# Optimization experiments

Hardware: AMD Instinct MI355X
Metric: run time of the kernel (lower is better)

Reference implementation:

```python
import jax, jax.numpy as jnp
import numpy as np

B, T, D, H, NL, DFF = 8, 255, 1024, 16, 8, 4096
DH = D // H
STD = 0.02


def setup_inputs() -> dict:
    key = jax.random.key(0)
    ks = jax.random.split(key, 16)
    n = lambda k, shape, s=STD: jax.random.normal(k, shape, dtype=jnp.float32) * s
    return {
        "x": n(ks[0], (B, T, D), 1.0),
        "mask": jnp.ones((B, T), dtype=jnp.int64),
        "is_train": 0,
        "sum_emb": n(ks[1], (1, D)),
        "modality_emb": n(ks[2], (T + 1, D)),
        "ln1_w": jnp.ones((NL, D), jnp.float32),
        "ln1_b": jnp.zeros((NL, D), jnp.float32),
        "w_qkv": n(ks[3], (NL, D, 3 * D)),
        "b_qkv": jnp.zeros((NL, 3 * D), jnp.float32),
        "w_proj": n(ks[4], (NL, D, D), STD / np.sqrt(2 * NL)),
        "b_proj": jnp.zeros((NL, D), jnp.float32),
        "ln2_w": jnp.ones((NL, D), jnp.float32),
        "ln2_b": jnp.zeros((NL, D), jnp.float32),
        "w_fc": n(ks[5], (NL, D, DFF)),
        "b_fc": jnp.zeros((NL, DFF), jnp.float32),
        "w_out": n(ks[6], (NL, DFF, D), STD / np.sqrt(2 * NL)),
        "b_out": jnp.zeros((NL, D), jnp.float32),
        "norm_w": jnp.ones((D,), jnp.float32),
        "norm_b": jnp.zeros((D,), jnp.float32),
    }


def _ln(x, w, b, eps=1e-5):
    m = x.mean(-1, keepdims=True)
    v = ((x - m) ** 2).mean(-1, keepdims=True)
    return (x - m) / jnp.sqrt(v + eps) * w + b


def reference(x, mask, is_train, sum_emb, modality_emb, ln1_w, ln1_b, w_qkv, b_qkv,
              w_proj, b_proj, ln2_w, ln2_b, w_fc, b_fc, w_out, b_out, norm_w, norm_b):
    b, t, d = x.shape
    L = t + 1
    # prepend summary token + its mask bit, add modality (position) embedding
    summ = jnp.broadcast_to(sum_emb[None, :, :], (b, 1, d))
    h = jnp.concatenate([summ, x], axis=1) + modality_emb[None, :, :]  # [B,L,D]
    full_mask = jnp.concatenate([jnp.ones((b, 1), mask.dtype), mask], axis=1)  # [B,L]
    key_bias = jnp.where(full_mask[:, None, None, :] == 1, 0.0, -1e9)  # [B,1,1,L]
    # is_train==0: random input-drop loop is a no-op in eval mode

    def block(h, p):
        l1w, l1b, wq, bq, wp, bp, l2w, l2b, wf, bf, wo, bo = p
        a = _ln(h, l1w, l1b)
        qkv = a @ wq + bq
        q, k, v = jnp.split(qkv, 3, axis=-1)
        q = q.reshape(b, L, H, DH).transpose(0, 2, 1, 3)
        k = k.reshape(b, L, H, DH).transpose(0, 2, 1, 3)
        v = v.reshape(b, L, H, DH).transpose(0, 2, 1, 3)
        scores = jnp.einsum("bhqd,bhkd->bhqk", q, k) / np.sqrt(DH) + key_bias
        att = jax.nn.softmax(scores, axis=-1)  # [B,H,L,L]
        y = jnp.einsum("bhqk,bhkd->bhqd", att, v).transpose(0, 2, 1, 3).reshape(b, L, d)
        h = h + y @ wp + bp
        m = _ln(h, l2w, l2b)
        h = h + jax.nn.gelu(m @ wf + bf) @ wo + bo
        return h, att

    params = (ln1_w, ln1_b, w_qkv, b_qkv, w_proj, b_proj, ln2_w, ln2_b, w_fc, b_fc, w_out, b_out)
    h, all_att = jax.lax.scan(block, h, params)
    h = _ln(h, norm_w, norm_b)
    return h[:, 0], all_att
```

## Files before the change

kernel.cpp:

```cpp
#include <hip/hip_runtime.h>


using u16 = unsigned short;
typedef __attribute__((ext_vector_type(8))) __bf16 bf16x8;
typedef __attribute__((ext_vector_type(4))) float f32x4;
typedef __attribute__((ext_vector_type(8))) unsigned short ushort8;

__device__ __forceinline__ u16 f2b(float f) {
  unsigned u = __builtin_bit_cast(unsigned, f);
  return (u16)((u + 0x7FFFu + ((u >> 16) & 1u)) >> 16);
}

__device__ __forceinline__ bf16x8 ldfrag(const u16* p) {
  return *reinterpret_cast<const bf16x8*>(p);
}

__device__ __forceinline__ f32x4 mfma16(bf16x8 a, bf16x8 b, f32x4 c) {
  return __builtin_amdgcn_mfma_f32_16x16x32_bf16(a, b, c, 0, 0, 0);
}

__device__ __forceinline__ void gload16(const void* g, void* l) {
  __builtin_amdgcn_global_load_lds(
      (const __attribute__((address_space(1))) unsigned int*)g,
      (__attribute__((address_space(3))) unsigned int*)l, 16, 0, 0);
}

__global__ __launch_bounds__(256) void embed_k(
    const float* __restrict__ x, const float* __restrict__ sum_emb,
    const float* __restrict__ mod_emb, float* __restrict__ h) {
  int idx = blockIdx.x * 256 + threadIdx.x;
  int d = idx & 1023;
  int l = (idx >> 10) & 255;
  int b = idx >> 18;
  float v = (l == 0) ? sum_emb[d] : x[(size_t)(b * 255 + l - 1) * 1024 + d];
  h[idx] = v + mod_emb[l * 1024 + d];
}

__global__ __launch_bounds__(256) void transpose_w(
    const float* __restrict__ in, u16* __restrict__ out, int R, int C) {
  __shared__ float tile[32][33];
  in += (size_t)blockIdx.z * R * C;
  out += (size_t)blockIdx.z * R * C;
  const int t = threadIdx.x;
  const int r0 = blockIdx.y * 32, c0 = blockIdx.x * 32;
  const int tr = t >> 5, tc = t & 31;
#pragma unroll
  for (int i = 0; i < 4; ++i)
    tile[tr + i * 8][tc] = in[(size_t)(r0 + tr + i * 8) * C + c0 + tc];
  __syncthreads();
#pragma unroll
  for (int i = 0; i < 4; ++i) {
    int cc = tr + i * 8, rr = tc;
    out[(size_t)(c0 + cc) * R + r0 + rr] = f2b(tile[rr][cc]);
  }
}

__global__ __launch_bounds__(256) void ln_bf16(
    const float* __restrict__ x, const float* __restrict__ w,
    const float* __restrict__ bb, u16* __restrict__ out) {
  const int r = blockIdx.x, t = threadIdx.x;
  const float* xr = x + (size_t)r * 1024;
  float v[4], s1 = 0.f, s2 = 0.f;
#pragma unroll
  for (int i = 0; i < 4; ++i) {
    v[i] = xr[t + i * 256];
    s1 += v[i];
    s2 += v[i] * v[i];
  }
#pragma unroll
  for (int o = 32; o > 0; o >>= 1) {
    s1 += __shfl_down(s1, o);
    s2 += __shfl_down(s2, o);
  }
  __shared__ float red[8];
  const int wv = t >> 6, l = t & 63;
  if (l == 0) { red[wv] = s1; red[4 + wv] = s2; }
  __syncthreads();
  s1 = red[0] + red[1] + red[2] + red[3];
  s2 = red[4] + red[5] + red[6] + red[7];
  float mean = s1 * (1.0f / 1024.0f);
  float var = s2 * (1.0f / 1024.0f) - mean * mean;
  float rstd = rsqrtf(var + 1e-5f);
#pragma unroll
  for (int i = 0; i < 4; ++i) {
    int c = t + i * 256;
    out[(size_t)r * 1024 + c] = f2b((v[i] - mean) * rstd * w[c] + bb[c]);
  }
}

__global__ __launch_bounds__(256) void final_ln(
    const float* __restrict__ h, const float* __restrict__ w,
    const float* __restrict__ bb, float* __restrict__ out) {
  const int r = blockIdx.x, t = threadIdx.x;
  const float* xr = h + (size_t)r * 262144;
  float v[4], s1 = 0.f, s2 = 0.f;
#pragma unroll
  for (int i = 0; i < 4; ++i) {
    v[i] = xr[t + i * 256];
    s1 += v[i];
    s2 += v[i] * v[i];
  }
#pragma unroll
  for (int o = 32; o > 0; o >>= 1) {
    s1 += __shfl_down(s1, o);
    s2 += __shfl_down(s2, o);
  }
  __shared__ float red[8];
  const int wv = t >> 6, l = t & 63;
  if (l == 0) { red[wv] = s1; red[4 + wv] = s2; }
  __syncthreads();
  s1 = red[0] + red[1] + red[2] + red[3];
  s2 = red[4] + red[5] + red[6] + red[7];
  float mean = s1 * (1.0f / 1024.0f);
  float var = s2 * (1.0f / 1024.0f) - mean * mean;
  float rstd = rsqrtf(var + 1e-5f);
#pragma unroll
  for (int i = 0; i < 4; ++i) {
    int c = t + i * 256;
    out[r * 1024 + c] = (v[i] - mean) * rstd * w[c] + bb[c];
  }
}

template <int EPI, int SPLIT>
__global__ __launch_bounds__(256) void gemm_bt(
    const u16* __restrict__ A, const u16* __restrict__ BT,
    const float* __restrict__ bias, float* __restrict__ Hres,
    u16* __restrict__ Obf, int M, int N, int K) {
  __shared__ u16 As[128 * 32];
  __shared__ u16 Bs[128 * 32];
  const int t = threadIdx.x;
  const int m0 = blockIdx.y * 128, n0 = blockIdx.x * 128;
  const int Kl = K / SPLIT;
  const int kz = (SPLIT > 1) ? blockIdx.z : 0;
  A += (size_t)kz * Kl;
  BT += (size_t)kz * Kl;
  const int l = t & 63, w = t >> 6;
  const int wr = (w >> 1) * 64, wc = (w & 1) * 64;
  const int lr = l & 15, lh = l >> 4;

  const int srow = t >> 2;
  const int skc = (t & 3) * 8;
  const u16* Ag = A + (size_t)(m0 + srow) * K + skc;
  const u16* Bg = BT + (size_t)(n0 + srow) * K + skc;

  f32x4 acc[4][4] = {};
  const int nk = Kl / 32;
  for (int kt = 0; kt < nk; ++kt) {
    __syncthreads();
    gload16(Ag, As + t * 8);
    gload16(Ag + (size_t)64 * K, As + 2048 + t * 8);
    gload16(Bg, Bs + t * 8);
    gload16(Bg + (size_t)64 * K, Bs + 2048 + t * 8);
    Ag += 32;
    Bg += 32;
    __syncthreads();
    bf16x8 af[4], bfr[4];
#pragma unroll
    for (int m = 0; m < 4; ++m) af[m] = ldfrag(As + (wr + m * 16 + lr) * 32 + lh * 8);
#pragma unroll
    for (int n = 0; n < 4; ++n) bfr[n] = ldfrag(Bs + (wc + n * 16 + lr) * 32 + lh * 8);
#pragma unroll
    for (int m = 0; m < 4; ++m)
#pragma unroll
      for (int n = 0; n < 4; ++n) acc[m][n] = mfma16(af[m], bfr[n], acc[m][n]);
  }
#pragma unroll
  for (int m = 0; m < 4; ++m) {
#pragma unroll
    for (int n = 0; n < 4; ++n) {
      const int col = n0 + wc + n * 16 + lr;
      const float bc = (SPLIT == 1 || kz == 0) ? bias[col] : 0.0f;
#pragma unroll
      for (int j = 0; j < 4; ++j) {
        const int row = m0 + wr + m * 16 + lh * 4 + j;
        float v = acc[m][n][j] + bc;
        if (EPI == 0) {
          Obf[(size_t)row * N + col] = f2b(v);
        } else if (EPI == 1) {
          size_t idx = (size_t)row * N + col;
          if (SPLIT == 1) Hres[idx] = Hres[idx] + v;
          else atomicAdd(Hres + idx, v);
        } else {
          float g = 0.5f * v *
                    (1.0f + tanhf(0.7978845608028654f * (v + 0.044715f * v * v * v)));
          Obf[(size_t)row * N + col] = f2b(g);
        }
      }
    }
  }
}

#define VS 264
__device__ __forceinline__ int sfi(int row, int col) {
  return row * 256 + ((col & 7) | (((col >> 3) ^ (row & 7)) << 3));
}

__global__ __launch_bounds__(256) void attn_fused(
    const u16* __restrict__ qkv, const int* __restrict__ mask,
    float* __restrict__ att_out, u16* __restrict__ y) {
  __shared__ u16 Qs[32 * 64];
  __shared__ u16 KV[64 * VS];
  __shared__ float Sf[32 * 256];
  __shared__ float mbias[256];
  __shared__ float rmax[32], rsum[32];
  const int t = threadIdx.x;
  const int blk = blockIdx.x;
  const int qt = blk & 7, hh = (blk >> 3) & 15, b = blk >> 7;
  const int q0 = qt * 32;

  mbias[t] = (t == 0) ? 0.0f : ((mask[b * 255 + t - 1] == 1) ? 0.0f : -1e9f);

  {
    int row = t >> 3, c = t & 7;
    int gcol = (c ^ (row & 7)) * 8;
    gload16(qkv + (size_t)(b * 256 + q0 + row) * 3072 + hh * 64 + gcol, Qs + t * 8);
  }
#pragma unroll
  for (int s = 0; s < 8; ++s) {
    int row = s * 32 + (t >> 3), c = t & 7;
    int gcol = (c ^ (row & 7)) * 8;
    gload16(qkv + (size_t)(b * 256 + row) * 3072 + 1024 + hh * 64 + gcol,
            KV + s * 2048 + t * 8);
  }
  __syncthreads();

  const int l = t & 63, w = t >> 6;
  const int lr = l & 15, lh = l >> 4;
  {
    const int c0 = w * 64;
    f32x4 acc[2][4] = {};
#pragma unroll
    for (int ks = 0; ks < 2; ++ks) {
      bf16x8 af[2], bfr[4];
#pragma unroll
      for (int m = 0; m < 2; ++m) {
        int row = m * 16 + lr;
        int chunk = (ks * 4 + lh) ^ (row & 7);
        af[m] = ldfrag(Qs + row * 64 + chunk * 8);
      }
#pragma unroll
      for (int n = 0; n < 4; ++n) {
        int row = c0 + n * 16 + lr;
        int chunk = (ks * 4 + lh) ^ (row & 7);
        bfr[n] = ldfrag(KV + row * 64 + chunk * 8);
      }
#pragma unroll
      for (int m = 0; m < 2; ++m)
#pragma unroll
        for (int n = 0; n < 4; ++n) acc[m][n] = mfma16(af[m], bfr[n], acc[m][n]);
    }
#pragma unroll
    for (int m = 0; m < 2; ++m)
#pragma unroll
      for (int n = 0; n < 4; ++n) {
        const int col = c0 + n * 16 + lr;
        const float mb = mbias[col];
#pragma unroll
        for (int j = 0; j < 4; ++j) {
          int row = m * 16 + lh * 4 + j;
          Sf[sfi(row, col)] = acc[m][n][j] * 0.125f + mb;
        }
      }
  }
  __syncthreads();

  ushort8 vreg[4][2];
#pragma unroll
  for (int s = 0; s < 4; ++s) {
    const int j = s * 64 + (t >> 2);
    const u16* vsrc =
        qkv + (size_t)(b * 256 + j) * 3072 + 2048 + hh * 64 + (t & 3) * 16;
    vreg[s][0] = *reinterpret_cast<const ushort8*>(vsrc);
    vreg[s][1] = *reinterpret_cast<const ushort8*>(vsrc + 8);
  }

  {
    const int row = t >> 3, tg = t & 7;
    float mx = -1e30f;
#pragma unroll 8
    for (int k = 0; k < 32; ++k) mx = fmaxf(mx, Sf[sfi(row, tg * 32 + k)]);
    mx = fmaxf(mx, __shfl_xor(mx, 1));
    mx = fmaxf(mx, __shfl_xor(mx, 2));
    mx = fmaxf(mx, __shfl_xor(mx, 4));
    float sm = 0.f;
#pragma unroll 8
    for (int k = 0; k < 32; ++k) sm += __expf(Sf[sfi(row, tg * 32 + k)] - mx);
    sm += __shfl_xor(sm, 1);
    sm += __shfl_xor(sm, 2);
    sm += __shfl_xor(sm, 4);
    if (tg == 0) {
      rmax[row] = mx;
      rsum[row] = 1.0f / sm;
    }
  }

#pragma unroll
  for (int s = 0; s < 4; ++s) {
    const int j = s * 64 + (t >> 2);
    const int d0 = (t & 3) * 16;
#pragma unroll
    for (int e = 0; e < 8; ++e) {
      KV[(d0 + e) * VS + j] = vreg[s][0][e];
      KV[(d0 + 8 + e) * VS + j] = vreg[s][1][e];
    }
  }
  __syncthreads();

  const size_t obase = ((size_t)b * 16 + hh) * 65536 + (size_t)q0 * 256;
#pragma unroll 4
  for (int i = 0; i < 32; ++i) {
    float p = __expf(Sf[sfi(i, t)] - rmax[i]) * rsum[i];
    att_out[obase + (size_t)i * 256 + t] = p;
  }

  {
    const int mrow = (w & 1) * 16;
    const int n0c = (w >> 1) * 32;
    const int rr = mrow + lr;
    const float mxl = rmax[rr], rsl = rsum[rr];
    f32x4 acc2[2] = {};
#pragma unroll
    for (int ks = 0; ks < 8; ++ks) {
      const int kbase = ks * 32 + lh * 8;
      const int ch = (kbase >> 3) ^ (rr & 7);
      const float* sp = &Sf[rr * 256 + ch * 8];
      f32x4 s0 = *reinterpret_cast<const f32x4*>(sp);
      f32x4 s1 = *reinterpret_cast<const f32x4*>(sp + 4);
      ushort8 pu;
#pragma unroll
      for (int e = 0; e < 4; ++e) pu[e] = f2b(__expf(s0[e] - mxl) * rsl);
#pragma unroll
      for (int e = 0; e < 4; ++e) pu[4 + e] = f2b(__expf(s1[e] - mxl) * rsl);
      bf16x8 af = __builtin_bit_cast(bf16x8, pu);
#pragma unroll
      for (int n = 0; n < 2; ++n) {
        bf16x8 bfr = ldfrag(KV + (n0c + n * 16 + lr) * VS + kbase);
        acc2[n] = mfma16(af, bfr, acc2[n]);
      }
    }
#pragma unroll
    for (int n = 0; n < 2; ++n)
#pragma unroll
      for (int j = 0; j < 4; ++j) {
        int row = mrow + lh * 4 + j;
        int col = n0c + n * 16 + lr;
        y[(size_t)(b * 256 + q0 + row) * 1024 + hh * 64 + col] = f2b(acc2[n][j]);
      }
  }
}

extern "C" void kernel_launch(void* const* d_in, const int* in_sizes, int n_in,
                              void* d_out, int out_size, void* d_ws, size_t ws_size,
                              hipStream_t stream) {
  (void)in_sizes; (void)n_in; (void)out_size;
  const float* x      = (const float*)d_in[0];
  const int* mask     = (const int*)d_in[1];
  const float* sum_emb = (const float*)d_in[3];
  const float* mod_emb = (const float*)d_in[4];
  const float* ln1_w  = (const float*)d_in[5];
  const float* ln1_b  = (const float*)d_in[6];
  const float* w_qkv  = (const float*)d_in[7];
  const float* b_qkv  = (const float*)d_in[8];
  const float* w_proj = (const float*)d_in[9];
  const float* b_proj = (const float*)d_in[10];
  const float* ln2_w  = (const float*)d_in[11];
  const float* ln2_b  = (const float*)d_in[12];
  const float* w_fc   = (const float*)d_in[13];
  const float* b_fc   = (const float*)d_in[14];
  const float* w_out  = (const float*)d_in[15];
  const float* b_out  = (const float*)d_in[16];
  const float* norm_w = (const float*)d_in[17];
  const float* norm_b = (const float*)d_in[18];

  char* ws = (char*)d_ws;
  float* h    = (float*)(ws + 0);
  u16* a_bf   = (u16*)(ws + 8388608);
  u16* qkv_bf = (u16*)(ws + 12582912);
  u16* y_bf   = (u16*)(ws + 25165824);
  u16* g_bf   = (u16*)(ws + 29360128);
  u16* wqkvT  = (u16*)(ws + 46137344);
  u16* wprojT = (u16*)(ws + 96468992);
  u16* wfcT   = (u16*)(ws + 113246208);
  u16* woutT  = (u16*)(ws + 180355072);
  float* att_f = (float*)d_out + 8192;

  const bool big = ws_size >= 248000000ull;
  const size_t stq = big ? (size_t)3072 * 1024 : 0;
  const size_t stp = big ? (size_t)1024 * 1024 : 0;
  const size_t stf = big ? (size_t)4096 * 1024 : 0;
  const size_t sto = big ? (size_t)4096 * 1024 : 0;

  embed_k<<<8192, 256, 0, stream>>>(x, sum_emb, mod_emb, h);

  if (big) {
    transpose_w<<<dim3(96, 32, 8), 256, 0, stream>>>(w_qkv, wqkvT, 1024, 3072);
    transpose_w<<<dim3(32, 32, 8), 256, 0, stream>>>(w_proj, wprojT, 1024, 1024);
    transpose_w<<<dim3(128, 32, 8), 256, 0, stream>>>(w_fc, wfcT, 1024, 4096);
    transpose_w<<<dim3(32, 128, 8), 256, 0, stream>>>(w_out, woutT, 4096, 1024);
  }

  for (int L = 0; L < 8; ++L) {
    if (!big) {
      transpose_w<<<dim3(96, 32, 1), 256, 0, stream>>>(
          w_qkv + (size_t)L * 1024 * 3072, wqkvT, 1024, 3072);
      transpose_w<<<dim3(32, 32, 1), 256, 0, stream>>>(
          w_proj + (size_t)L * 1024 * 1024, wprojT, 1024, 1024);
      transpose_w<<<dim3(128, 32, 1), 256, 0, stream>>>(
          w_fc + (size_t)L * 1024 * 4096, wfcT, 1024, 4096);
      transpose_w<<<dim3(32, 128, 1), 256, 0, stream>>>(
          w_out + (size_t)L * 4096 * 1024, woutT, 4096, 1024);
    }
    ln_bf16<<<2048, 256, 0, stream>>>(h, ln1_w + L * 1024, ln1_b + L * 1024, a_bf);
    gemm_bt<0, 1><<<dim3(24, 16, 1), 256, 0, stream>>>(
        a_bf, wqkvT + L * stq, b_qkv + L * 3072, nullptr, qkv_bf, 2048, 3072, 1024);
    attn_fused<<<1024, 256, 0, stream>>>(qkv_bf, mask,
                                         att_f + (size_t)L * 8388608, y_bf);
    gemm_bt<1, 2><<<dim3(8, 16, 2), 256, 0, stream>>>(
        y_bf, wprojT + L * stp, b_proj + L * 1024, h, nullptr, 2048, 1024, 1024);
    ln_bf16<<<2048, 256, 0, stream>>>(h, ln2_w + L * 1024, ln2_b + L * 1024, a_bf);
    gemm_bt<2, 1><<<dim3(32, 16, 1), 256, 0, stream>>>(
        a_bf, wfcT + L * stf, b_fc + L * 4096, nullptr, g_bf, 2048, 4096, 1024);
    gemm_bt<1, 4><<<dim3(8, 16, 4), 256, 0, stream>>>(
        g_bf, woutT + L * sto, b_out + L * 1024, h, nullptr, 2048, 1024, 4096);
  }

  final_ln<<<8, 256, 0, stream>>>(h, norm_w, norm_b, (float*)d_out);
}
```

Before: 2.110 ms.

## Rewrite GEMM with double-buffered LDS, 128x256 tiles, XOR swizzle and grid remap

The GEMM kernel is replaced by a 512-thread version that computes 128x256 output tiles with a K-step of 64. It double-buffers the LDS tiles so the next tile's global-to-LDS loads overlap the current MFMAs, and drops one barrier per iteration. Shared-memory columns are XOR-swizzled to avoid bank conflicts, and block IDs are remapped in groups of 8 for better cache locality. The proj GEMM moves from split-K 2 to split-K 4, which means more atomics. The larger tiles also raise LDS use to about 96KB and reduce the number of blocks per GEMM.

```diff
diff --git a/kernel.cpp b/kernel.cpp
--- a/kernel.cpp
+++ b/kernel.cpp
@@ -122,57 +122,84 @@
 }
 
 template <int EPI, int SPLIT>
-__global__ __launch_bounds__(256) void gemm_bt(
+__global__ __launch_bounds__(512) void gemm2p(
     const u16* __restrict__ A, const u16* __restrict__ BT,
     const float* __restrict__ bias, float* __restrict__ Hres,
     u16* __restrict__ Obf, int M, int N, int K) {
-  __shared__ u16 As[128 * 32];
-  __shared__ u16 Bs[128 * 32];
+  __shared__ u16 As[2][128 * 64];
+  __shared__ u16 Bs[2][256 * 64];
   const int t = threadIdx.x;
-  const int m0 = blockIdx.y * 128, n0 = blockIdx.x * 128;
+  const int gx = gridDim.x, nwg = gx * gridDim.y;
+  int id = blockIdx.y * gx + blockIdx.x;
+  id = (id & 7) * (nwg >> 3) + (id >> 3);
+  const int m0 = (id / gx) * 128, n0 = (id % gx) * 256;
+
   const int Kl = K / SPLIT;
   const int kz = (SPLIT > 1) ? blockIdx.z : 0;
   A += (size_t)kz * Kl;
   BT += (size_t)kz * Kl;
+
   const int l = t & 63, w = t >> 6;
-  const int wr = (w >> 1) * 64, wc = (w & 1) * 64;
+  const int wm = w >> 2, wn = w & 3;
   const int lr = l & 15, lh = l >> 4;
 
-  const int srow = t >> 2;
-  const int skc = (t & 3) * 8;
-  const u16* Ag = A + (size_t)(m0 + srow) * K + skc;
-  const u16* Bg = BT + (size_t)(n0 + srow) * K + skc;
+  const int sr = t >> 3, sc = t & 7;
+  const int scA = (sc ^ (sr & 7)) * 8;
 
   f32x4 acc[4][4] = {};
-  const int nk = Kl / 32;
+  const int nk = Kl / 64;
+  int cur = 0;
+
+#define STAGE_TILE(bb, kt)                                                     \
+  {                                                                            \
+    const size_t kof = (size_t)(kt)*64 + scA;                                  \
+    gload16(A + (size_t)(m0 + sr) * K + kof, &As[bb][t * 8]);                  \
+    gload16(A + (size_t)(m0 + sr + 64) * K + kof, &As[bb][4096 + t * 8]);      \
+    gload16(BT + (size_t)(n0 + sr) * K + kof, &Bs[bb][t * 8]);                 \
+    gload16(BT + (size_t)(n0 + sr + 64) * K + kof, &Bs[bb][4096 + t * 8]);     \
+    gload16(BT + (size_t)(n0 + sr + 128) * K + kof, &Bs[bb][8192 + t * 8]);    \
+    gload16(BT + (size_t)(n0 + sr + 192) * K + kof, &Bs[bb][12288 + t * 8]);   \
+  }
+
+  STAGE_TILE(0, 0);
+  __syncthreads();
+
   for (int kt = 0; kt < nk; ++kt) {
+    if (kt + 1 < nk) STAGE_TILE(cur ^ 1, kt + 1);
+    bf16x8 af[4][2], bfr[4][2];
+#pragma unroll
+    for (int ks = 0; ks < 2; ++ks) {
+#pragma unroll
+      for (int m = 0; m < 4; ++m) {
+        const int row = wm * 64 + m * 16 + lr;
+        af[m][ks] = ldfrag(&As[cur][row * 64 + (((ks * 4 + lh) ^ (row & 7)) << 3)]);
+      }
+#pragma unroll
+      for (int n = 0; n < 4; ++n) {
+        const int row = wn * 64 + n * 16 + lr;
+        bfr[n][ks] = ldfrag(&Bs[cur][row * 64 + (((ks * 4 + lh) ^ (row & 7)) << 3)]);
+      }
+    }
+#pragma unroll
+    for (int ks = 0; ks < 2; ++ks)
+#pragma unroll
+      for (int m = 0; m < 4; ++m)
+#pragma unroll
+        for (int n = 0; n < 4; ++n) acc[m][n] = mfma16(af[m][ks], bfr[n][ks], acc[m][n]);
     __syncthreads();
-    gload16(Ag, As + t * 8);
-    gload16(Ag + (size_t)64 * K, As + 2048 + t * 8);
-    gload16(Bg, Bs + t * 8);
-    gload16(Bg + (size_t)64 * K, Bs + 2048 + t * 8);
-    Ag += 32;
-    Bg += 32;
-    __syncthreads();
-    bf16x8 af[4], bfr[4];
-#pragma unroll
-    for (int m = 0; m < 4; ++m) af[m] = ldfrag(As + (wr + m * 16 + lr) * 32 + lh * 8);
-#pragma unroll
-    for (int n = 0; n < 4; ++n) bfr[n] = ldfrag(Bs + (wc + n * 16 + lr) * 32 + lh * 8);
-#pragma unroll
-    for (int m = 0; m < 4; ++m)
-#pragma unroll
-      for (int n = 0; n < 4; ++n) acc[m][n] = mfma16(af[m], bfr[n], acc[m][n]);
-  }
+    cur ^= 1;
+  }
+#undef STAGE_TILE
+
 #pragma unroll
   for (int m = 0; m < 4; ++m) {
 #pragma unroll
     for (int n = 0; n < 4; ++n) {
-      const int col = n0 + wc + n * 16 + lr;
+      const int col = n0 + wn * 64 + n * 16 + lr;
       const float bc = (SPLIT == 1 || kz == 0) ? bias[col] : 0.0f;
 #pragma unroll
       for (int j = 0; j < 4; ++j) {
-        const int row = m0 + wr + m * 16 + lh * 4 + j;
+        const int row = m0 + wm * 64 + m * 16 + lh * 4 + j;
         float v = acc[m][n][j] + bc;
         if (EPI == 0) {
           Obf[(size_t)row * N + col] = f2b(v);
@@ -411,16 +438,16 @@
           w_out + (size_t)L * 4096 * 1024, woutT, 4096, 1024);
     }
     ln_bf16<<<2048, 256, 0, stream>>>(h, ln1_w + L * 1024, ln1_b + L * 1024, a_bf);
-    gemm_bt<0, 1><<<dim3(24, 16, 1), 256, 0, stream>>>(
+    gemm2p<0, 1><<<dim3(12, 16, 1), 512, 0, stream>>>(
         a_bf, wqkvT + L * stq, b_qkv + L * 3072, nullptr, qkv_bf, 2048, 3072, 1024);
     attn_fused<<<1024, 256, 0, stream>>>(qkv_bf, mask,
                                          att_f + (size_t)L * 8388608, y_bf);
-    gemm_bt<1, 2><<<dim3(8, 16, 2), 256, 0, stream>>>(
+    gemm2p<1, 4><<<dim3(4, 16, 4), 512, 0, stream>>>(
         y_bf, wprojT + L * stp, b_proj + L * 1024, h, nullptr, 2048, 1024, 1024);
     ln_bf16<<<2048, 256, 0, stream>>>(h, ln2_w + L * 1024, ln2_b + L * 1024, a_bf);
-    gemm_bt<2, 1><<<dim3(32, 16, 1), 256, 0, stream>>>(
+    gemm2p<2, 1><<<dim3(16, 16, 1), 512, 0, stream>>>(
         a_bf, wfcT + L * stf, b_fc + L * 4096, nullptr, g_bf, 2048, 4096, 1024);
-    gemm_bt<1, 4><<<dim3(8, 16, 4), 256, 0, stream>>>(
+    gemm2p<1, 4><<<dim3(4, 16, 4), 512, 0, stream>>>(
         g_bf, woutT + L * sto, b_out + L * 1024, h, nullptr, 2048, 1024, 4096);
   }
 
```

After: 2.100 ms. About the same (-0.5%).
